# Kernel optimization log

Measured on AMD Instinct MI355X. Metric: run time of the kernel, lower is better.

## Reference

```python
import jax, jax.numpy as jnp
import numpy as np

C_IN = 256
C_BN = 64


def conv1x1(x, w, b):
    # x: [B, Cin, H, W], w: [Cout, Cin], b: [Cout] -> [B, Cout, H, W]
    return jnp.einsum('oc,bchw->bohw', w, x) + b[None, :, None, None]


def setup_inputs() -> dict:
    key = jax.random.key(0)
    ks = jax.random.split(key, 9)
    B, H, W = 4, 64, 64
    s_in = 1.0 / np.sqrt(C_IN)
    s_bn = 1.0 / np.sqrt(C_BN)
    return {
        'x': jax.random.normal(ks[0], (B, C_IN, H, W), jnp.float32),
        'w_k': jax.random.uniform(ks[1], (C_BN, C_IN), jnp.float32, -s_in, s_in),
        'b_k': jax.random.uniform(ks[2], (C_BN,), jnp.float32, -s_in, s_in),
        'w_q': jax.random.uniform(ks[3], (C_BN, C_IN), jnp.float32, -s_in, s_in),
        'b_q': jax.random.uniform(ks[4], (C_BN,), jnp.float32, -s_in, s_in),
        'w_v': jax.random.uniform(ks[5], (C_BN, C_IN), jnp.float32, -s_in, s_in),
        'b_v': jax.random.uniform(ks[6], (C_BN,), jnp.float32, -s_in, s_in),
        'w_u': jax.random.uniform(ks[7], (C_IN, C_BN), jnp.float32, -s_bn, s_bn),
        'b_u': jax.random.uniform(ks[8], (C_IN,), jnp.float32, -s_bn, s_bn),
    }


def reference(x, w_k, b_k, w_q, b_q, w_v, b_v, w_u, b_u):
    B, C, H, W = x.shape
    N = H * W
    xk = conv1x1(x, w_k, b_k).reshape(B, C_BN, N)            # [B, d, N]
    xq = conv1x1(x, w_q, b_q).reshape(B, C_BN, N)            # [B, d, N]
    xv = conv1x1(x, w_v, b_v).reshape(B, C_BN, N)            # [B, d, N]
    qk = jnp.einsum('bdi,bdk->bik', xq, xk)                  # [B, N, N]
    attn = jax.nn.softmax(qk, axis=2)                        # softmax over keys
    out = jnp.einsum('bik,bdk->bdi', attn, xv)               # [B, d, N]
    out = out.reshape(B, C_BN, H, W)
    y = conv1x1(out, w_u, b_u)                               # [B, C, H, W]
    return x + y
```

## Files before the change

kernel.cpp:

```cpp
#include <hip/hip_runtime.h>
#include <math.h>

#define N_TOK 4096
#define CIN 256
#define CBN 64
#define LOG2E 1.44269504f

typedef __attribute__((ext_vector_type(8))) short bf16x8;
typedef __attribute__((ext_vector_type(4))) float f32x4;

static __device__ __forceinline__ unsigned short f2bf(float f) {
    union { float f; unsigned u; } v; v.f = f;
    unsigned r = v.u + 0x7fffu + ((v.u >> 16) & 1u);
    return (unsigned short)(r >> 16);
}
static __device__ __forceinline__ unsigned pack2(float a, float b) {
    return (unsigned)f2bf(a) | ((unsigned)f2bf(b) << 16);
}

__global__ __launch_bounds__(256) void prep_w(
        const float* __restrict__ wq, const float* __restrict__ wk,
        const float* __restrict__ wv, const float* __restrict__ wu,
        const float* __restrict__ bq,
        short* __restrict__ Wb, short* __restrict__ Wu, float* __restrict__ bqs) {
    int idx = blockIdx.x * 256 + threadIdx.x;
    int d = idx >> 8, c = idx & 255;
    Wb[d * 256 + c]         = (short)f2bf(wq[idx] * LOG2E);
    Wb[(64 + d) * 256 + c]  = (short)f2bf(wk[idx]);
    Wb[(128 + d) * 256 + c] = (short)f2bf(wv[idx]);
    Wu[idx] = (short)f2bf(wu[idx]);
    if (idx < 64) bqs[idx] = bq[idx] * LOG2E;
}

__global__ __launch_bounds__(256) void qkv_kernel(
        const float* __restrict__ x, const short* __restrict__ Wb,
        const float* __restrict__ bqs, const float* __restrict__ bk, const float* __restrict__ bv,
        short* __restrict__ Qt, short* __restrict__ Kt, short* __restrict__ Vd) {
    int t = threadIdx.x;
    int blk = blockIdx.x;
    int b = blk >> 7;
    int n0 = (blk & 127) * 32;

    __shared__ short Xs[32][264];

    {
        int tok4 = t & 7;
        int cb = t >> 3;
        const float* xb = x + (size_t)b * CIN * N_TOK + n0 + tok4 * 4;
        #pragma unroll
        for (int p = 0; p < 8; ++p) {
            int c = p * 32 + cb;
            float4 xv = *(const float4*)(xb + (size_t)c * N_TOK);
            float xs[4] = {xv.x, xv.y, xv.z, xv.w};
            #pragma unroll
            for (int i = 0; i < 4; ++i)
                Xs[tok4 * 4 + i][c] = (short)f2bf(xs[i]);
        }
    }
    __syncthreads();

    int w = t >> 6;
    int g = (t >> 4) & 3;
    int lr = t & 15;

    f32x4 acc[3][2];
    #pragma unroll
    for (int m = 0; m < 3; ++m)
        #pragma unroll
        for (int st = 0; st < 2; ++st) acc[m][st] = (f32x4){0.f, 0.f, 0.f, 0.f};
    const short* wbase = Wb + (size_t)(w * 16 + lr) * 256 + 8 * g;
    #pragma unroll
    for (int ks = 0; ks < 8; ++ks) {
        bf16x8 xf0 = *(const bf16x8*)&Xs[lr][ks * 32 + 8 * g];
        bf16x8 xf1 = *(const bf16x8*)&Xs[16 + lr][ks * 32 + 8 * g];
        #pragma unroll
        for (int m = 0; m < 3; ++m) {
            bf16x8 wf = *(const bf16x8*)(wbase + (size_t)m * 64 * 256 + ks * 32);
            acc[m][0] = __builtin_amdgcn_mfma_f32_16x16x32_bf16(wf, xf0, acc[m][0], 0, 0, 0);
            acc[m][1] = __builtin_amdgcn_mfma_f32_16x16x32_bf16(wf, xf1, acc[m][1], 0, 0, 0);
        }
    }
    int d0 = w * 16 + 4 * g;
    float4 bq4 = *(const float4*)(bqs + d0);
    float4 bk4 = *(const float4*)(bk + d0);
    float4 bv4 = *(const float4*)(bv + d0);
    float bvr[4] = {bv4.x, bv4.y, bv4.z, bv4.w};
    #pragma unroll
    for (int st = 0; st < 2; ++st) {
        int tok = n0 + st * 16 + lr;
        size_t qo = ((size_t)b * N_TOK + tok) * 64 + d0;
        uint2 qp, kp;
        qp.x = pack2(acc[0][st][0] + bq4.x, acc[0][st][1] + bq4.y);
        qp.y = pack2(acc[0][st][2] + bq4.z, acc[0][st][3] + bq4.w);
        kp.x = pack2(acc[1][st][0] + bk4.x, acc[1][st][1] + bk4.y);
        kp.y = pack2(acc[1][st][2] + bk4.z, acc[1][st][3] + bk4.w);
        *(uint2*)(Qt + qo) = qp;
        *(uint2*)(Kt + qo) = kp;
        int u = tok & 31;
        int vcol = (tok & ~31) + 8 * ((u >> 2) & 3) + 4 * (u >> 4) + (u & 3);
        #pragma unroll
        for (int r = 0; r < 4; ++r)
            Vd[((size_t)b * 64 + d0 + r) * N_TOK + vcol] = (short)f2bf(acc[2][st][r] + bvr[r]);
    }
}

__global__ __launch_bounds__(1024, 4) void attn_kernel(
        const short* __restrict__ Qt, const short* __restrict__ Kt,
        const short* __restrict__ Vsw, short* __restrict__ Otm) {
    int t = threadIdx.x;
    int w = t >> 6;
    int wq = w >> 3;
    int sp = w & 7;
    int g = (t >> 4) & 3;
    int lr = t & 15;
    int l = t & 63;

    int bid = blockIdx.x;
    int blk = ((bid & 7) << 5) | (bid >> 3);
    int b = blk >> 6;
    int q0 = (blk & 63) * 64;

    const short* Qb = Qt + (size_t)b * N_TOK * 64;
    const short* Kb = Kt + (size_t)b * N_TOK * 64;
    const short* Vb = Vsw + (size_t)b * 64 * N_TOK;

    __shared__ __align__(16) char LB[8][2][8192];
    __shared__ float Ml[32][16];

    bf16x8 qf[2][2];
    #pragma unroll
    for (int j = 0; j < 2; ++j) {
        const short* qp = Qb + (q0 + (wq * 2 + j) * 16 + lr) * 64 + 8 * g;
        qf[j][0] = *(const bf16x8*)qp;
        qf[j][1] = *(const bf16x8*)(qp + 32);
    }

    f32x4 o[2][4];
    #pragma unroll
    for (int j = 0; j < 2; ++j)
        #pragma unroll
        for (int mt = 0; mt < 4; ++mt) o[j][mt] = (f32x4){0.f, 0.f, 0.f, 0.f};
    float la0 = 0.f, la1 = 0.f;

    int krow = l >> 3;
    int kchk = ((l & 7) ^ krow) * 8;
    int vrow = l >> 2;
    int vchk = ((l & 3) ^ (vrow & 3)) * 8;

    auto STAGE = [&](int kt, int buf) {
        int k0s = sp * 512 + kt * 32;
        char* dst0 = &LB[sp][buf][0];
        if (wq == 0) {
            #pragma unroll
            for (int j = 0; j < 4; ++j) {
                const short* src = Kb + (size_t)(k0s + j * 8 + krow) * 64 + kchk;
                __builtin_amdgcn_global_load_lds(
                    (const __attribute__((address_space(1))) void*)src,
                    (__attribute__((address_space(3))) void*)(dst0 + j * 1024),
                    16, 0, 0);
            }
        } else {
            #pragma unroll
            for (int j = 0; j < 4; ++j) {
                const short* src = Vb + (size_t)(j * 16 + vrow) * N_TOK + k0s + vchk;
                __builtin_amdgcn_global_load_lds(
                    (const __attribute__((address_space(1))) void*)src,
                    (__attribute__((address_space(3))) void*)(dst0 + 4096 + j * 1024),
                    16, 0, 0);
            }
        }
    };

    STAGE(0, 0);
    __syncthreads();

    int cK = (g ^ (lr & 7)) << 4;
    int cV = (g ^ (lr & 3)) << 4;
    int cur = 0;
    for (int kt = 0; kt < 16; ++kt) {
        if (kt < 15) STAGE(kt + 1, cur ^ 1);
        const char* KB_ = &LB[sp][cur][0];
        const char* VB_ = KB_ + 4096;
        f32x4 s[2][2];
        #pragma unroll
        for (int nt = 0; nt < 2; ++nt) {
            const char* rp = KB_ + (nt * 16 + lr) * 128;
            bf16x8 kf0 = *(const bf16x8*)(rp + cK);
            bf16x8 kf1 = *(const bf16x8*)(rp + (cK ^ 64));
            #pragma unroll
            for (int j = 0; j < 2; ++j) {
                f32x4 z = (f32x4){0.f, 0.f, 0.f, 0.f};
                z = __builtin_amdgcn_mfma_f32_16x16x32_bf16(kf0, qf[j][0], z, 0, 0, 0);
                s[j][nt] = __builtin_amdgcn_mfma_f32_16x16x32_bf16(kf1, qf[j][1], z, 0, 0, 0);
            }
        }
        #pragma unroll
        for (int nt = 0; nt < 2; ++nt)
            #pragma unroll
            for (int r = 0; r < 4; ++r) {
                float p0 = __builtin_amdgcn_exp2f(s[0][nt][r]);
                float p1 = __builtin_amdgcn_exp2f(s[1][nt][r]);
                s[0][nt][r] = p0; la0 += p0;
                s[1][nt][r] = p1; la1 += p1;
            }
        bf16x8 bp[2];
        #pragma unroll
        for (int e = 0; e < 8; ++e) {
            bp[0][e] = (short)f2bf(s[0][e >> 2][e & 3]);
            bp[1][e] = (short)f2bf(s[1][e >> 2][e & 3]);
        }
        #pragma unroll
        for (int mt = 0; mt < 4; ++mt) {
            bf16x8 av = *(const bf16x8*)(VB_ + (mt * 16 + lr) * 64 + cV);
            o[0][mt] = __builtin_amdgcn_mfma_f32_16x16x32_bf16(av, bp[0], o[0][mt], 0, 0, 0);
            o[1][mt] = __builtin_amdgcn_mfma_f32_16x16x32_bf16(av, bp[1], o[1][mt], 0, 0, 0);
        }
        __syncthreads();
        cur ^= 1;
    }
    la0 += __shfl_xor(la0, 16); la0 += __shfl_xor(la0, 32);
    la1 += __shfl_xor(la1, 16); la1 += __shfl_xor(la1, 32);
    float* OmL = (float*)&LB[0][0][0];
    #pragma unroll
    for (int j = 0; j < 2; ++j) {
        int qt = wq * 2 + j;
        #pragma unroll
        for (int mt = 0; mt < 4; ++mt)
            *(f32x4*)(OmL + ((qt * 8 + sp) * 16 + lr) * 64 + mt * 16 + 4 * g) = o[j][mt];
        Ml[qt * 8 + sp][lr] = j == 0 ? la0 : la1;
    }
    __syncthreads();
    {
        int qt2 = t >> 8, q = (t >> 4) & 15, dq = t & 15;
        float a0 = 0.f, a1 = 0.f, a2 = 0.f, a3 = 0.f, lsum = 0.f;
        #pragma unroll
        for (int s2 = 0; s2 < 8; ++s2) {
            const float* pp = OmL + ((qt2 * 8 + s2) * 16 + q) * 64 + dq * 4;
            float4 v = *(const float4*)pp;
            a0 += v.x; a1 += v.y; a2 += v.z; a3 += v.w;
            lsum += Ml[qt2 * 8 + s2][q];
        }
        float inv = 1.f / lsum;
        int tok = q0 + qt2 * 16 + q;
        uint2 ow;
        ow.x = pack2(a0 * inv, a1 * inv);
        ow.y = pack2(a2 * inv, a3 * inv);
        *(uint2*)(Otm + ((size_t)b * N_TOK + tok) * 64 + dq * 4) = ow;
    }
}

__global__ __launch_bounds__(256) void out_kernel(
        const short* __restrict__ Otm, const short* __restrict__ Wu,
        const float* __restrict__ bu, const float* __restrict__ x,
        float* __restrict__ y) {
    int t = threadIdx.x;
    int w = t >> 6, g = (t >> 4) & 3, lr = t & 15;
    int blk = blockIdx.x;
    int b = blk >> 8;
    int rem = blk & 255;
    int nblk = rem >> 2, cblk = rem & 3;
    int n0 = nblk * 64 + w * 16;
    int c0 = cblk * 64;

    const short* Ob = Otm + ((size_t)b * N_TOK + n0) * 64;
    bf16x8 a0 = *(const bf16x8*)(Ob + lr * 64 + 8 * g);
    bf16x8 a1 = *(const bf16x8*)(Ob + lr * 64 + 32 + 8 * g);

    #pragma unroll
    for (int ct = 0; ct < 4; ++ct) {
        int c = c0 + ct * 16 + lr;
        const short* wp = Wu + (size_t)c * 64 + 8 * g;
        bf16x8 b0 = *(const bf16x8*)wp;
        bf16x8 b1 = *(const bf16x8*)(wp + 32);
        f32x4 acc = (f32x4){0.f, 0.f, 0.f, 0.f};
        acc = __builtin_amdgcn_mfma_f32_16x16x32_bf16(a0, b0, acc, 0, 0, 0);
        acc = __builtin_amdgcn_mfma_f32_16x16x32_bf16(a1, b1, acc, 0, 0, 0);
        float bc = bu[c];
        size_t base = ((size_t)b * CIN + c) * N_TOK + n0 + 4 * g;
        float4 xr = *(const float4*)(x + base);
        float4 yo;
        yo.x = acc[0] + bc + xr.x;
        yo.y = acc[1] + bc + xr.y;
        yo.z = acc[2] + bc + xr.z;
        yo.w = acc[3] + bc + xr.w;
        *(float4*)(y + base) = yo;
    }
}

extern "C" void kernel_launch(void* const* d_in, const int* in_sizes, int n_in,
                              void* d_out, int out_size, void* d_ws, size_t ws_size,
                              hipStream_t stream) {
    const float* x  = (const float*)d_in[0];
    const float* wk = (const float*)d_in[1];
    const float* bk = (const float*)d_in[2];
    const float* wq = (const float*)d_in[3];
    const float* bq = (const float*)d_in[4];
    const float* wv = (const float*)d_in[5];
    const float* bv = (const float*)d_in[6];
    const float* wu = (const float*)d_in[7];
    const float* bu = (const float*)d_in[8];
    float* out = (float*)d_out;

    char* ws = (char*)d_ws;
    if (ws_size < (size_t)(9u << 20)) return;
    short* Qt  = (short*)(ws);
    short* Kt  = (short*)(ws + (2u << 20));
    short* Vd  = (short*)(ws + (4u << 20));
    short* Otm = (short*)(ws + (6u << 20));
    short* Wb  = (short*)(ws + (8u << 20));
    short* Wu  = Wb + 192 * 256;
    float* bqs = (float*)(Wu + 256 * 64);

    prep_w<<<dim3(64), dim3(256), 0, stream>>>(wq, wk, wv, wu, bq, Wb, Wu, bqs);
    qkv_kernel<<<dim3(512), dim3(256), 0, stream>>>(x, Wb, bqs, bk, bv, Qt, Kt, Vd);
    attn_kernel<<<dim3(256), dim3(1024), 0, stream>>>(Qt, Kt, Vd, Otm);
    out_kernel<<<dim3(1024), dim3(256), 0, stream>>>(Otm, Wu, bu, x, out);
}
```

Baseline: 61.79 us.

## Fuse output 1x1 conv into attention kernel and use packed bf16 conversion

The separate out_kernel is removed. Each attention block now writes its normalized 64x64 output tile into swizzled LDS and immediately runs the up-projection MFMA, bias add and residual add, writing the final fp32 output directly. This drops one launch and the global round trip of the intermediate O tensor. Separately, the hand-written bf16 rounding in pack2 is replaced by the HIP packed float2-to-bfloat162 intrinsic, which may map to a native convert instruction in the hot P-packing path. The trade-off is extra LDS, a tail phase inside the attention kernel, and only 256 blocks doing the output GEMM instead of 1024.

```diff
diff --git a/kernel.cpp b/kernel.cpp
--- a/kernel.cpp
+++ b/kernel.cpp
@@ -1,4 +1,5 @@
 #include <hip/hip_runtime.h>
+#include <hip/hip_bf16.h>
 #include <math.h>
 
 #define N_TOK 4096
@@ -15,7 +16,10 @@
     return (unsigned short)(r >> 16);
 }
 static __device__ __forceinline__ unsigned pack2(float a, float b) {
-    return (unsigned)f2bf(a) | ((unsigned)f2bf(b) << 16);
+    float2 t2; t2.x = a; t2.y = b;
+    __hip_bfloat162 h = __float22bfloat162_rn(t2);
+    union { __hip_bfloat162 h; unsigned u; } cv; cv.h = h;
+    return cv.u;
 }
 
 __global__ __launch_bounds__(256) void prep_w(
@@ -104,9 +108,11 @@
     }
 }
 
-__global__ __launch_bounds__(1024, 4) void attn_kernel(
+__global__ __launch_bounds__(1024, 4) void attn_out_kernel(
         const short* __restrict__ Qt, const short* __restrict__ Kt,
-        const short* __restrict__ Vsw, short* __restrict__ Otm) {
+        const short* __restrict__ Vsw, const short* __restrict__ Wu,
+        const float* __restrict__ bu, const float* __restrict__ x,
+        float* __restrict__ y) {
     int t = threadIdx.x;
     int w = t >> 6;
     int wq = w >> 3;
@@ -126,6 +132,7 @@
 
     __shared__ __align__(16) char LB[8][2][8192];
     __shared__ float Ml[32][16];
+    __shared__ __align__(16) short Olds[64 * 64];
 
     bf16x8 qf[2][2];
     #pragma unroll
@@ -203,17 +210,20 @@
                 s[0][nt][r] = p0; la0 += p0;
                 s[1][nt][r] = p1; la1 += p1;
             }
-        bf16x8 bp[2];
-        #pragma unroll
-        for (int e = 0; e < 8; ++e) {
-            bp[0][e] = (short)f2bf(s[0][e >> 2][e & 3]);
-            bp[1][e] = (short)f2bf(s[1][e >> 2][e & 3]);
-        }
+        union { bf16x8 v; unsigned u[4]; } b0u, b1u;
+        b0u.u[0] = pack2(s[0][0][0], s[0][0][1]);
+        b0u.u[1] = pack2(s[0][0][2], s[0][0][3]);
+        b0u.u[2] = pack2(s[0][1][0], s[0][1][1]);
+        b0u.u[3] = pack2(s[0][1][2], s[0][1][3]);
+        b1u.u[0] = pack2(s[1][0][0], s[1][0][1]);
+        b1u.u[1] = pack2(s[1][0][2], s[1][0][3]);
+        b1u.u[2] = pack2(s[1][1][0], s[1][1][1]);
+        b1u.u[3] = pack2(s[1][1][2], s[1][1][3]);
         #pragma unroll
         for (int mt = 0; mt < 4; ++mt) {
             bf16x8 av = *(const bf16x8*)(VB_ + (mt * 16 + lr) * 64 + cV);
-            o[0][mt] = __builtin_amdgcn_mfma_f32_16x16x32_bf16(av, bp[0], o[0][mt], 0, 0, 0);
-            o[1][mt] = __builtin_amdgcn_mfma_f32_16x16x32_bf16(av, bp[1], o[1][mt], 0, 0, 0);
+            o[0][mt] = __builtin_amdgcn_mfma_f32_16x16x32_bf16(av, b0u.v, o[0][mt], 0, 0, 0);
+            o[1][mt] = __builtin_amdgcn_mfma_f32_16x16x32_bf16(av, b1u.v, o[1][mt], 0, 0, 0);
         }
         __syncthreads();
         cur ^= 1;
@@ -241,49 +251,40 @@
             lsum += Ml[qt2 * 8 + s2][q];
         }
         float inv = 1.f / lsum;
-        int tok = q0 + qt2 * 16 + q;
+        int tau = qt2 * 16 + q;
         uint2 ow;
         ow.x = pack2(a0 * inv, a1 * inv);
         ow.y = pack2(a2 * inv, a3 * inv);
-        *(uint2*)(Otm + ((size_t)b * N_TOK + tok) * 64 + dq * 4) = ow;
-    }
-}
-
-__global__ __launch_bounds__(256) void out_kernel(
-        const short* __restrict__ Otm, const short* __restrict__ Wu,
-        const float* __restrict__ bu, const float* __restrict__ x,
-        float* __restrict__ y) {
-    int t = threadIdx.x;
-    int w = t >> 6, g = (t >> 4) & 3, lr = t & 15;
-    int blk = blockIdx.x;
-    int b = blk >> 8;
-    int rem = blk & 255;
-    int nblk = rem >> 2, cblk = rem & 3;
-    int n0 = nblk * 64 + w * 16;
-    int c0 = cblk * 64;
-
-    const short* Ob = Otm + ((size_t)b * N_TOK + n0) * 64;
-    bf16x8 a0 = *(const bf16x8*)(Ob + lr * 64 + 8 * g);
-    bf16x8 a1 = *(const bf16x8*)(Ob + lr * 64 + 32 + 8 * g);
-
-    #pragma unroll
-    for (int ct = 0; ct < 4; ++ct) {
-        int c = c0 + ct * 16 + lr;
-        const short* wp = Wu + (size_t)c * 64 + 8 * g;
-        bf16x8 b0 = *(const bf16x8*)wp;
-        bf16x8 b1 = *(const bf16x8*)(wp + 32);
-        f32x4 acc = (f32x4){0.f, 0.f, 0.f, 0.f};
-        acc = __builtin_amdgcn_mfma_f32_16x16x32_bf16(a0, b0, acc, 0, 0, 0);
-        acc = __builtin_amdgcn_mfma_f32_16x16x32_bf16(a1, b1, acc, 0, 0, 0);
-        float bc = bu[c];
-        size_t base = ((size_t)b * CIN + c) * N_TOK + n0 + 4 * g;
-        float4 xr = *(const float4*)(x + base);
-        float4 yo;
-        yo.x = acc[0] + bc + xr.x;
-        yo.y = acc[1] + bc + xr.y;
-        yo.z = acc[2] + bc + xr.z;
-        yo.w = acc[3] + bc + xr.w;
-        *(float4*)(y + base) = yo;
+        char* dst = (char*)Olds + tau * 128 + (((dq >> 1) ^ (tau & 7)) << 4) + (dq & 1) * 8;
+        *(uint2*)dst = ow;
+    }
+    __syncthreads();
+    {
+        int tt = w & 3;
+        int cq = w >> 2;
+        int tau = tt * 16 + lr;
+        const char* orow = (const char*)Olds + tau * 128;
+        bf16x8 a0 = *(const bf16x8*)(orow + ((g ^ (lr & 7)) << 4));
+        bf16x8 a1 = *(const bf16x8*)(orow + (((4 + g) ^ (lr & 7)) << 4));
+        #pragma unroll
+        for (int ct = 0; ct < 4; ++ct) {
+            int c = cq * 64 + ct * 16 + lr;
+            const short* wp = Wu + (size_t)c * 64 + 8 * g;
+            bf16x8 b0 = *(const bf16x8*)wp;
+            bf16x8 b1 = *(const bf16x8*)(wp + 32);
+            f32x4 acc = (f32x4){0.f, 0.f, 0.f, 0.f};
+            acc = __builtin_amdgcn_mfma_f32_16x16x32_bf16(a0, b0, acc, 0, 0, 0);
+            acc = __builtin_amdgcn_mfma_f32_16x16x32_bf16(a1, b1, acc, 0, 0, 0);
+            float bc = bu[c];
+            size_t base = ((size_t)b * CIN + c) * N_TOK + q0 + tt * 16 + 4 * g;
+            float4 xr = *(const float4*)(x + base);
+            float4 yo;
+            yo.x = acc[0] + bc + xr.x;
+            yo.y = acc[1] + bc + xr.y;
+            yo.z = acc[2] + bc + xr.z;
+            yo.w = acc[3] + bc + xr.w;
+            *(float4*)(y + base) = yo;
+        }
     }
 }
 
@@ -302,17 +303,15 @@
     float* out = (float*)d_out;
 
     char* ws = (char*)d_ws;
-    if (ws_size < (size_t)(9u << 20)) return;
+    if (ws_size < (size_t)(7u << 20)) return;
     short* Qt  = (short*)(ws);
     short* Kt  = (short*)(ws + (2u << 20));
     short* Vd  = (short*)(ws + (4u << 20));
-    short* Otm = (short*)(ws + (6u << 20));
-    short* Wb  = (short*)(ws + (8u << 20));
+    short* Wb  = (short*)(ws + (6u << 20));
     short* Wu  = Wb + 192 * 256;
     float* bqs = (float*)(Wu + 256 * 64);
 
     prep_w<<<dim3(64), dim3(256), 0, stream>>>(wq, wk, wv, wu, bq, Wb, Wu, bqs);
     qkv_kernel<<<dim3(512), dim3(256), 0, stream>>>(x, Wb, bqs, bk, bv, Qt, Kt, Vd);
-    attn_kernel<<<dim3(256), dim3(1024), 0, stream>>>(Qt, Kt, Vd, Otm);
-    out_kernel<<<dim3(1024), dim3(256), 0, stream>>>(Otm, Wu, bu, x, out);
-}
+    attn_out_kernel<<<dim3(256), dim3(1024), 0, stream>>>(Qt, Kt, Vd, Wu, bu, x, out);
+}
```

Result: faster. 58.78 us (-4.9%).
